# Kernel optimization log

Hardware: AMD Instinct MI355X
Metric: run time of the kernel (lower is better)

The kernel has to match this reference:

```python
import jax, jax.numpy as jnp
import numpy as np

ANCHORS = np.array([[10,13],[16,30],[33,23],[30,61],[62,45],[59,119],[116,90],[156,198],[373,326]], np.float32)
ANCHOR_MASK = [[6, 7, 8], [3, 4, 5], [0, 1, 2]]
INPUT_SHAPE = np.array([416, 416], np.float32)  # (h, w)
NUM_CLASSES = 80
EPS = 1e-7


def _bce(pred, target):
    # clip_by_tensor + binary cross entropy, as in the torch module
    p = jnp.clip(pred, EPS, 1.0 - EPS)
    return -target * jnp.log(p) - (1.0 - target) * jnp.log(1.0 - p)


def _box_iou(b1, b2):
    # b1: (..., 1, 4), b2: (..., n, 4), center-format xywh (normalized)
    b1_xy, b1_wh = b1[..., :2], b1[..., 2:4]
    b2_xy, b2_wh = b2[..., :2], b2[..., 2:4]
    b1_min, b1_max = b1_xy - b1_wh / 2.0, b1_xy + b1_wh / 2.0
    b2_min, b2_max = b2_xy - b2_wh / 2.0, b2_xy + b2_wh / 2.0
    inter_wh = jnp.maximum(jnp.minimum(b1_max, b2_max) - jnp.maximum(b1_min, b2_min), 0.0)
    inter = inter_wh[..., 0] * inter_wh[..., 1]
    a1 = b1_wh[..., 0] * b1_wh[..., 1]
    a2 = b2_wh[..., 0] * b2_wh[..., 1]
    return inter / (a1 + a2 - inter)


def _decode(y_pred, anchors):
    # y_pred: (b, 3*(5+C), h, w) -> raw: (b, 3, h, w, 5+C)
    b, _, h, w = y_pred.shape
    raw = y_pred.reshape(b, 3, 5 + NUM_CLASSES, h, w).transpose(0, 1, 3, 4, 2)
    gy, gx = jnp.meshgrid(jnp.arange(h, dtype=y_pred.dtype), jnp.arange(w, dtype=y_pred.dtype), indexing='ij')
    grid_xy = jnp.stack([gx, gy], axis=-1)  # (h, w, 2)
    pred_xy = jax.nn.sigmoid(raw[..., 0:2])
    pred_wh = raw[..., 2:4]                 # raw tw, th (MSE'd against log target)
    pred_conf = jax.nn.sigmoid(raw[..., 4:5])
    pred_class = jax.nn.sigmoid(raw[..., 5:])
    # decoded, normalized boxes for IoU-based negative mining
    box_xy = (pred_xy + grid_xy) / jnp.array([w, h], y_pred.dtype)
    box_wh = jnp.exp(pred_wh) * anchors.reshape(3, 1, 1, 2) / jnp.asarray(INPUT_SHAPE[::-1].copy())
    pred_box = jnp.concatenate([box_xy, box_wh], axis=-1)  # (b,3,h,w,4)
    return grid_xy, pred_box, pred_xy, pred_wh, pred_conf, pred_class


def _layer_loss(y_pred, y_true, target, anchors):
    b, _, h, w = y_pred.shape
    grid_xy, pred_box, pred_xy, pred_wh, pred_conf, pred_class = _decode(y_pred, anchors)
    object_mask = y_true[..., 4:5]
    true_xy = y_true[..., 0:2] * jnp.array([h, w], y_pred.dtype) - grid_xy
    true_wh = jnp.log(y_true[..., 2:4] * jnp.asarray(INPUT_SHAPE[::-1].copy()) / anchors.reshape(3, 1, 1, 2))
    true_wh = jnp.where(object_mask > 0, true_wh, jnp.zeros_like(true_wh))
    loss_scale = 2.0 - y_true[..., 2:3] * y_true[..., 3:4]
    # negative mask: every grid/anchor prediction vs all true boxes of its image (vectorized over batch)
    iou = _box_iou(pred_box[:, :, :, :, None, :], target[:, None, None, None, :, :4])  # (b,3,h,w,n)
    best_iou = jnp.max(iou, axis=-1)
    neg = (best_iou < 0.5).astype(y_pred.dtype)[..., None]
    neg_mask = (1.0 - object_mask) * neg
    loss_xy = jnp.sum(object_mask * loss_scale * _bce(pred_xy, true_xy))
    loss_wh = jnp.sum(object_mask * loss_scale * 0.5 * (pred_wh - true_wh) ** 2)
    conf_bce = _bce(pred_conf, object_mask)
    loss_conf = jnp.sum(object_mask * conf_bce) + jnp.sum(neg_mask * conf_bce)
    loss_cls = jnp.sum(object_mask * _bce(pred_class, y_true[..., 5:]))
    return loss_xy + loss_wh + loss_conf + loss_cls


def setup_inputs() -> dict:
    key = jax.random.key(0)
    ks = jax.random.split(key, 7)
    grids = [13, 26, 52]
    b, n = 32, 20
    inp = {}
    for i, g in enumerate(grids):
        inp[f'y_pred{i}'] = jax.random.normal(ks[i], (b, 3 * (5 + NUM_CLASSES), g, g), jnp.float32)
        # y_true values in (0.05, 0.95): keeps log(true_wh) and 1/y_true grads bounded
        inp[f'y_true{i}'] = 0.05 + 0.9 * jax.random.uniform(ks[3 + i], (b, 3, g, g, 5 + NUM_CLASSES), jnp.float32)
    inp['target'] = 0.05 + 0.9 * jax.random.uniform(ks[6], (b, n, 5), jnp.float32)
    return inp


def reference(y_pred0, y_pred1, y_pred2, y_true0, y_true1, y_true2, target):
    total = jnp.zeros((), jnp.float32)
    for yp, yt, mask in ((y_pred0, y_true0, ANCHOR_MASK[0]),
                         (y_pred1, y_true1, ANCHOR_MASK[1]),
                         (y_pred2, y_true2, ANCHOR_MASK[2])):
        total = total + _layer_loss(yp, yt, target, jnp.asarray(ANCHORS[mask]))
    return total
```

## Files before the change

kernel.cpp:

```cpp
#include <hip/hip_runtime.h>
#include <math.h>

#define BLOCK 256
#define NB0 64
#define NB1 254
#define NB2 1014
#define NBLOCKS (NB0 + NB1 + NB2)

__constant__ float c_anch[9][2] = {
    {116.f, 90.f}, {156.f, 198.f}, {373.f, 326.f},
    { 30.f, 61.f}, { 62.f,  45.f}, { 59.f, 119.f},
    { 10.f, 13.f}, { 16.f,  30.f}, { 33.f,  23.f}
};

__device__ __forceinline__ float softplusf(float x) {
    float ax = fabsf(x);
    return fmaxf(x, 0.f) + __logf(1.f + __expf(-ax));
}

__device__ __forceinline__ float sigmoidf(float x) {
    return __fdividef(1.f, 1.f + __expf(-x));
}

__global__ __launch_bounds__(BLOCK) void yolo_loss_main(
    const float* __restrict__ p0, const float* __restrict__ p1, const float* __restrict__ p2,
    const float* __restrict__ t0, const float* __restrict__ t1, const float* __restrict__ t2,
    const float* __restrict__ tgt, float* __restrict__ out)
{
    int blk = blockIdx.x;
    const float* pred;
    const float* tru;
    int layer, g, cells, bbase;
    if (blk < NB0)            { layer = 0; pred = p0; tru = t0; g = 13; cells = 16224;  bbase = 0; }
    else if (blk < NB0 + NB1) { layer = 1; pred = p1; tru = t1; g = 26; cells = 64896;  bbase = NB0; }
    else                      { layer = 2; pred = p2; tru = t2; g = 52; cells = 259584; bbase = NB0 + NB1; }

    const int tid  = threadIdx.x;
    const int w    = tid >> 6;
    const int lane = tid & 63;
    const int cellbase = (blk - bbase) * BLOCK;
    const int wbase = cellbase + w * 64;
    const int idx   = wbase + lane;
    const bool valid = idx < cells;

    __shared__ float lds[4][16][68];

    const int hw = g * g;
    const float* pb = pred;
    float aw = 1.f, ah = 1.f, gx = 0.f, gy = 0.f;
    int b = 0;
    if (valid) {
        int ij = idx % hw;
        int a  = (idx / hw) % 3;
        b      = idx / (3 * hw);
        int i  = ij / g;
        int j  = ij - i * g;
        pb = pred + (size_t)((b * 3 + a) * 85) * hw + ij;
        aw = c_anch[layer * 3 + a][0];
        ah = c_anch[layer * 3 + a][1];
        gx = (float)j; gy = (float)i;
    }
    const float gf = (float)g;

    const float* src = tru + (size_t)wbase * 85;

    float acc = 0.f;
    float cls = 0.f;
    float mask = 0.f;

#pragma unroll
    for (int k = 0; k < 16; k++) {
        int e  = k * 64 + lane;
        int cl = e >> 4, c = e & 15;
        if (wbase + cl < cells)
            lds[w][c][cl] = src[(size_t)cl * 85 + c];
    }

    if (valid) {
        float y0 = lds[w][0][lane], y1 = lds[w][1][lane];
        float y2 = lds[w][2][lane], y3 = lds[w][3][lane];
        mask = lds[w][4][lane];

        float r0 = pb[0];
        float r1 = pb[hw];
        float r2 = pb[2 * hw];
        float r3 = pb[3 * hw];
        float r4 = pb[4 * hw];

        float true_x = y0 * gf - gx;
        float true_y = y1 * gf - gy;
        float ls = 2.f - y2 * y3;
        float lxy = (softplusf(r0) - true_x * r0) + (softplusf(r1) - true_y * r1);
        acc += mask * ls * lxy;

        float tw = __logf(y2 * (416.f / aw));
        float th = __logf(y3 * (416.f / ah));
        float dw = r2 - tw, dh = r3 - th;
        acc += mask * ls * 0.5f * (dw * dw + dh * dh);

        float cbce = softplusf(r4) - mask * r4;
        float sx = sigmoidf(r0);
        float sy = sigmoidf(r1);
        float bx = __fdividef(sx + gx, gf);
        float by = __fdividef(sy + gy, gf);
        float bw = __expf(r2) * aw * (1.f / 416.f);
        float bh = __expf(r3) * ah * (1.f / 416.f);
        float a1 = bw * bh;
        float b1minx = bx - 0.5f * bw, b1maxx = bx + 0.5f * bw;
        float b1miny = by - 0.5f * bh, b1maxy = by + 0.5f * bh;

        const float* tg = tgt + b * 20 * 5;
        float best = 0.f;
#pragma unroll 4
        for (int k = 0; k < 20; k++) {
            float tx  = tg[k * 5 + 0];
            float ty  = tg[k * 5 + 1];
            float tww = tg[k * 5 + 2];
            float thh = tg[k * 5 + 3];
            float iw = fminf(b1maxx, tx + 0.5f * tww) - fmaxf(b1minx, tx - 0.5f * tww);
            float ih = fminf(b1maxy, ty + 0.5f * thh) - fmaxf(b1miny, ty - 0.5f * thh);
            iw = fmaxf(iw, 0.f);
            ih = fmaxf(ih, 0.f);
            float inter = iw * ih;
            float iou = __fdividef(inter, a1 + tww * thh - inter);
            best = fmaxf(best, iou);
        }
        float neg = (best < 0.5f) ? 1.f : 0.f;
        acc += mask * cbce + (1.f - mask) * neg * cbce;

#pragma unroll
        for (int c = 5; c < 16; c++) {
            float x = pb[c * hw];
            float t = lds[w][c][lane];
            cls += softplusf(x) - t * x;
        }
    }

#pragma unroll
    for (int c0 = 16; c0 < 80; c0 += 16) {
#pragma unroll
        for (int k = 0; k < 16; k++) {
            int e  = k * 64 + lane;
            int cl = e >> 4, c = e & 15;
            if (wbase + cl < cells)
                lds[w][c][cl] = src[(size_t)cl * 85 + c0 + c];
        }
        if (valid) {
#pragma unroll
            for (int c = 0; c < 16; c++) {
                float x = pb[(c0 + c) * hw];
                float t = lds[w][c][lane];
                cls += softplusf(x) - t * x;
            }
        }
    }

#pragma unroll
    for (int k = 0; k < 5; k++) {
        int e  = k * 64 + lane;
        int cl = e / 5, c = e - cl * 5;
        if (wbase + cl < cells)
            lds[w][c][cl] = src[(size_t)cl * 85 + 80 + c];
    }
    if (valid) {
#pragma unroll
        for (int c = 0; c < 5; c++) {
            float x = pb[(80 + c) * hw];
            float t = lds[w][c][lane];
            cls += softplusf(x) - t * x;
        }
        acc += mask * cls;
    }

    for (int off = 32; off > 0; off >>= 1)
        acc += __shfl_down(acc, off, 64);
    __shared__ float sh[BLOCK / 64];
    if (lane == 0)
        sh[w] = acc;
    __syncthreads();
    if (tid == 0) {
        float s = 0.f;
        for (int wv = 0; wv < BLOCK / 64; wv++) s += sh[wv];
        atomicAdd(out, s);
    }
}

extern "C" void kernel_launch(void* const* d_in, const int* in_sizes, int n_in,
                              void* d_out, int out_size, void* d_ws, size_t ws_size,
                              hipStream_t stream) {
    const float* p0  = (const float*)d_in[0];
    const float* t0  = (const float*)d_in[1];
    const float* p1  = (const float*)d_in[2];
    const float* t1  = (const float*)d_in[3];
    const float* p2  = (const float*)d_in[4];
    const float* t2  = (const float*)d_in[5];
    const float* tgt = (const float*)d_in[6];

    hipMemsetAsync(d_out, 0, sizeof(float), stream);
    yolo_loss_main<<<NBLOCKS, BLOCK, 0, stream>>>(p0, p1, p2, t0, t1, t2, tgt, (float*)d_out);
}
```

Baseline: 301.7 us.

## Process four cells per lane with vectorized loads in single-wave blocks

Changes blocks to a single 64-lane wavefront in which each lane handles four consecutive cells of layers 1 and 2. Prediction planes are read with float4 loads, and y_true rows are staged through a transposing LDS tile using float4 reads. Layer 0 (13x13, where a 4-cell group can straddle plane boundaries) moves to a scalar per-thread path that reads y_true directly. The block-level LDS reduction and barrier are replaced by one atomic per wave, which raises the atomic count on the single output. The aim is wider memory transactions and amortized IoU target loads, at the cost of more registers per lane and more atomics.

```diff
diff --git a/kernel.cpp b/kernel.cpp
--- a/kernel.cpp
+++ b/kernel.cpp
@@ -1,11 +1,12 @@
 #include <hip/hip_runtime.h>
 #include <math.h>
 
-#define BLOCK 256
-#define NB0 64
-#define NB1 254
-#define NB2 1014
-#define NBLOCKS (NB0 + NB1 + NB2)
+typedef float f4 __attribute__((ext_vector_type(4)));
+
+#define NL2 1014
+#define NL1 254
+#define NL0 254
+#define NBLOCKS (NL2 + NL1 + NL0)
 
 __constant__ float c_anch[9][2] = {
     {116.f, 90.f}, {156.f, 198.f}, {373.f, 326.f},
@@ -17,172 +18,245 @@
     float ax = fabsf(x);
     return fmaxf(x, 0.f) + __logf(1.f + __expf(-ax));
 }
-
 __device__ __forceinline__ float sigmoidf(float x) {
     return __fdividef(1.f, 1.f + __expf(-x));
 }
 
-__global__ __launch_bounds__(BLOCK) void yolo_loss_main(
+__global__ __launch_bounds__(64) void yolo_loss_main(
     const float* __restrict__ p0, const float* __restrict__ p1, const float* __restrict__ p2,
     const float* __restrict__ t0, const float* __restrict__ t1, const float* __restrict__ t2,
     const float* __restrict__ tgt, float* __restrict__ out)
 {
-    int blk = blockIdx.x;
-    const float* pred;
-    const float* tru;
-    int layer, g, cells, bbase;
-    if (blk < NB0)            { layer = 0; pred = p0; tru = t0; g = 13; cells = 16224;  bbase = 0; }
-    else if (blk < NB0 + NB1) { layer = 1; pred = p1; tru = t1; g = 26; cells = 64896;  bbase = NB0; }
-    else                      { layer = 2; pred = p2; tru = t2; g = 52; cells = 259584; bbase = NB0 + NB1; }
-
-    const int tid  = threadIdx.x;
-    const int w    = tid >> 6;
-    const int lane = tid & 63;
-    const int cellbase = (blk - bbase) * BLOCK;
-    const int wbase = cellbase + w * 64;
-    const int idx   = wbase + lane;
-    const bool valid = idx < cells;
-
-    __shared__ float lds[4][16][68];
-
-    const int hw = g * g;
-    const float* pb = pred;
-    float aw = 1.f, ah = 1.f, gx = 0.f, gy = 0.f;
-    int b = 0;
-    if (valid) {
-        int ij = idx % hw;
-        int a  = (idx / hw) % 3;
-        b      = idx / (3 * hw);
-        int i  = ij / g;
-        int j  = ij - i * g;
-        pb = pred + (size_t)((b * 3 + a) * 85) * hw + ij;
-        aw = c_anch[layer * 3 + a][0];
-        ah = c_anch[layer * 3 + a][1];
-        gx = (float)j; gy = (float)i;
+    __shared__ float lds[16][260];
+
+    const int blk  = blockIdx.x;
+    const int lane = threadIdx.x;
+    float acc = 0.f;
+
+    if (blk < NL2 + NL1) {
+        const float* pred; const float* tru;
+        int hw, cells, base, arow;
+        int plane, ij0, cell0;
+        float gf;
+        float gxv[4], gyv[4];
+        if (blk < NL2) {
+            pred = p2; tru = t2; hw = 2704; cells = 259584; arow = 6; gf = 52.f;
+            base  = blk * 256;
+            cell0 = base + 4 * lane;
+            plane = cell0 / 2704; ij0 = cell0 - plane * 2704;
+#pragma unroll
+            for (int s = 0; s < 4; s++) { int ij = ij0 + s; int i = ij / 52; gyv[s] = (float)i; gxv[s] = (float)(ij - i * 52); }
+        } else {
+            pred = p1; tru = t1; hw = 676; cells = 64896; arow = 3; gf = 26.f;
+            base  = (blk - NL2) * 256;
+            cell0 = base + 4 * lane;
+            plane = cell0 / 676; ij0 = cell0 - plane * 676;
+#pragma unroll
+            for (int s = 0; s < 4; s++) { int ij = ij0 + s; int i = ij / 26; gyv[s] = (float)i; gxv[s] = (float)(ij - i * 26); }
+        }
+        const bool valid = cell0 < cells;
+        const int aIdx = plane % 3;
+        const int bIdx = plane / 3;
+        const float* pb = pred + (size_t)plane * 85 * hw + ij0;
+        const float aw = c_anch[arow + aIdx][0];
+        const float ah = c_anch[arow + aIdx][1];
+        const char* tbase = (const char*)tru + (size_t)base * 340;
+
+        f4 clsv = {0.f, 0.f, 0.f, 0.f};
+        float m4[4] = {0.f, 0.f, 0.f, 0.f};
+
+#pragma unroll
+        for (int k = 0; k < 16; k++) {
+            int u = k * 64 + lane;
+            int cell = u >> 2, q = u & 3;
+            if (base + cell < cells) {
+                f4 v = *(const f4*)(tbase + (size_t)cell * 340 + q * 16);
+                lds[4*q+0][cell] = v.x;
+                lds[4*q+1][cell] = v.y;
+                lds[4*q+2][cell] = v.z;
+                lds[4*q+3][cell] = v.w;
+            }
+        }
+        if (valid) {
+            f4 y0 = *(const f4*)&lds[0][4*lane];
+            f4 y1 = *(const f4*)&lds[1][4*lane];
+            f4 y2 = *(const f4*)&lds[2][4*lane];
+            f4 y3 = *(const f4*)&lds[3][4*lane];
+            f4 ym = *(const f4*)&lds[4][4*lane];
+            f4 r0 = *(const f4*)(pb);
+            f4 r1 = *(const f4*)(pb + (size_t)hw);
+            f4 r2 = *(const f4*)(pb + 2*(size_t)hw);
+            f4 r3 = *(const f4*)(pb + 3*(size_t)hw);
+            f4 r4 = *(const f4*)(pb + 4*(size_t)hw);
+
+            float cb[4], bminx[4], bmaxx[4], bminy[4], bmaxy[4], area[4], best[4];
+#pragma unroll
+            for (int s = 0; s < 4; s++) {
+                float R0 = r0[s], R1 = r1[s], R2 = r2[s], R3 = r3[s], R4 = r4[s];
+                float Y0 = y0[s], Y1 = y1[s], Y2 = y2[s], Y3 = y3[s], M = ym[s];
+                m4[s] = M;
+                float gx = gxv[s], gy = gyv[s];
+                float tx = Y0 * gf - gx, ty = Y1 * gf - gy;
+                float ls = 2.f - Y2 * Y3;
+                acc += M * ls * ((softplusf(R0) - tx * R0) + (softplusf(R1) - ty * R1));
+                float tw = __logf(Y2 * (416.f / aw));
+                float th = __logf(Y3 * (416.f / ah));
+                float dw = R2 - tw, dh = R3 - th;
+                acc += M * ls * 0.5f * (dw * dw + dh * dh);
+                cb[s] = softplusf(R4) - M * R4;
+                float sx = sigmoidf(R0), sy = sigmoidf(R1);
+                float bx = __fdividef(sx + gx, gf), by = __fdividef(sy + gy, gf);
+                float bw = __expf(R2) * aw * (1.f / 416.f);
+                float bh = __expf(R3) * ah * (1.f / 416.f);
+                area[s]  = bw * bh;
+                bminx[s] = bx - 0.5f * bw; bmaxx[s] = bx + 0.5f * bw;
+                bminy[s] = by - 0.5f * bh; bmaxy[s] = by + 0.5f * bh;
+                best[s]  = 0.f;
+            }
+            const float* tg = tgt + bIdx * 100;
+#pragma unroll 4
+            for (int k = 0; k < 20; k++) {
+                float tx = tg[5*k], ty = tg[5*k+1], tw = tg[5*k+2], th = tg[5*k+3];
+                float tminx = tx - 0.5f * tw, tmaxx = tx + 0.5f * tw;
+                float tminy = ty - 0.5f * th, tmaxy = ty + 0.5f * th;
+                float a2 = tw * th;
+#pragma unroll
+                for (int s = 0; s < 4; s++) {
+                    float iw = fmaxf(fminf(bmaxx[s], tmaxx) - fmaxf(bminx[s], tminx), 0.f);
+                    float ih = fmaxf(fminf(bmaxy[s], tmaxy) - fmaxf(bminy[s], tminy), 0.f);
+                    float inter = iw * ih;
+                    best[s] = fmaxf(best[s], __fdividef(inter, area[s] + a2 - inter));
+                }
+            }
+#pragma unroll
+            for (int s = 0; s < 4; s++) {
+                float neg = (best[s] < 0.5f) ? 1.f : 0.f;
+                acc += m4[s] * cb[s] + (1.f - m4[s]) * neg * cb[s];
+            }
+#pragma unroll
+            for (int c = 5; c < 16; c++) {
+                f4 tv = *(const f4*)&lds[c][4*lane];
+                f4 xv = *(const f4*)(pb + (size_t)c * hw);
+                f4 sp;
+                sp.x = softplusf(xv.x); sp.y = softplusf(xv.y);
+                sp.z = softplusf(xv.z); sp.w = softplusf(xv.w);
+                clsv += sp - tv * xv;
+            }
+        }
+
+        for (int cc = 16; cc < 80; cc += 16) {
+            const char* tc = tbase + cc * 4;
+#pragma unroll
+            for (int k = 0; k < 16; k++) {
+                int u = k * 64 + lane;
+                int cell = u >> 2, q = u & 3;
+                if (base + cell < cells) {
+                    f4 v = *(const f4*)(tc + (size_t)cell * 340 + q * 16);
+                    lds[4*q+0][cell] = v.x;
+                    lds[4*q+1][cell] = v.y;
+                    lds[4*q+2][cell] = v.z;
+                    lds[4*q+3][cell] = v.w;
+                }
+            }
+            if (valid) {
+#pragma unroll
+                for (int c = 0; c < 16; c++) {
+                    f4 tv = *(const f4*)&lds[c][4*lane];
+                    f4 xv = *(const f4*)(pb + (size_t)(cc + c) * hw);
+                    f4 sp;
+                    sp.x = softplusf(xv.x); sp.y = softplusf(xv.y);
+                    sp.z = softplusf(xv.z); sp.w = softplusf(xv.w);
+                    clsv += sp - tv * xv;
+                }
+            }
+        }
+
+        {
+            const char* tc = tbase + 320;
+#pragma unroll
+            for (int k = 0; k < 20; k++) {
+                int u = k * 64 + lane;
+                int cell = u / 5, c = u - cell * 5;
+                if (base + cell < cells)
+                    lds[c][cell] = *(const float*)(tc + (size_t)cell * 340 + c * 4);
+            }
+            if (valid) {
+#pragma unroll
+                for (int c = 0; c < 5; c++) {
+                    f4 tv = *(const f4*)&lds[c][4*lane];
+                    f4 xv = *(const f4*)(pb + (size_t)(80 + c) * hw);
+                    f4 sp;
+                    sp.x = softplusf(xv.x); sp.y = softplusf(xv.y);
+                    sp.z = softplusf(xv.z); sp.w = softplusf(xv.w);
+                    clsv += sp - tv * xv;
+                }
+            }
+        }
+
+        if (valid)
+            acc += m4[0]*clsv.x + m4[1]*clsv.y + m4[2]*clsv.z + m4[3]*clsv.w;
+
+    } else {
+        int t = (blk - NL2 - NL1) * 64 + lane;
+        if (t < 16224) {
+            int ij = t % 169;
+            int a  = (t / 169) % 3;
+            int b  = t / 507;
+            int i  = ij / 13;
+            int j  = ij - i * 13;
+            const float* pb = p0 + (size_t)((b * 3 + a) * 85) * 169 + ij;
+            const float* tb = t0 + (size_t)((b * 3 + a) * 169 + ij) * 85;
+
+            float r0 = pb[0], r1 = pb[169], r2 = pb[338], r3 = pb[507], r4 = pb[676];
+            float y0 = tb[0], y1 = tb[1], y2 = tb[2], y3 = tb[3], mask = tb[4];
+            float aw = c_anch[a][0], ah = c_anch[a][1];
+            float gx = (float)j, gy = (float)i;
+
+            float tx = y0 * 13.f - gx, ty = y1 * 13.f - gy;
+            float ls = 2.f - y2 * y3;
+            acc += mask * ls * ((softplusf(r0) - tx * r0) + (softplusf(r1) - ty * r1));
+            float tw = __logf(y2 * (416.f / aw));
+            float th = __logf(y3 * (416.f / ah));
+            float dw = r2 - tw, dh = r3 - th;
+            acc += mask * ls * 0.5f * (dw * dw + dh * dh);
+            float cbce = softplusf(r4) - mask * r4;
+
+            float sx = sigmoidf(r0), sy = sigmoidf(r1);
+            float bx = __fdividef(sx + gx, 13.f), by = __fdividef(sy + gy, 13.f);
+            float bw = __expf(r2) * aw * (1.f / 416.f);
+            float bh = __expf(r3) * ah * (1.f / 416.f);
+            float a1 = bw * bh;
+            float b1minx = bx - 0.5f * bw, b1maxx = bx + 0.5f * bw;
+            float b1miny = by - 0.5f * bh, b1maxy = by + 0.5f * bh;
+            const float* tg = tgt + b * 100;
+            float bestv = 0.f;
+#pragma unroll 4
+            for (int k = 0; k < 20; k++) {
+                float px = tg[5*k], py = tg[5*k+1], pw = tg[5*k+2], ph = tg[5*k+3];
+                float iw = fmaxf(fminf(b1maxx, px + 0.5f*pw) - fmaxf(b1minx, px - 0.5f*pw), 0.f);
+                float ih = fmaxf(fminf(b1maxy, py + 0.5f*ph) - fmaxf(b1miny, py - 0.5f*ph), 0.f);
+                float inter = iw * ih;
+                bestv = fmaxf(bestv, __fdividef(inter, a1 + pw * ph - inter));
+            }
+            float neg = (bestv < 0.5f) ? 1.f : 0.f;
+            acc += mask * cbce + (1.f - mask) * neg * cbce;
+
+            float cls = 0.f;
+#pragma unroll 8
+            for (int c = 0; c < 80; c++) {
+                float x = pb[(5 + c) * 169];
+                float tt = tb[5 + c];
+                cls += softplusf(x) - tt * x;
+            }
+            acc += mask * cls;
+        }
     }
-    const float gf = (float)g;
-
-    const float* src = tru + (size_t)wbase * 85;
-
-    float acc = 0.f;
-    float cls = 0.f;
-    float mask = 0.f;
-
-#pragma unroll
-    for (int k = 0; k < 16; k++) {
-        int e  = k * 64 + lane;
-        int cl = e >> 4, c = e & 15;
-        if (wbase + cl < cells)
-            lds[w][c][cl] = src[(size_t)cl * 85 + c];
-    }
-
-    if (valid) {
-        float y0 = lds[w][0][lane], y1 = lds[w][1][lane];
-        float y2 = lds[w][2][lane], y3 = lds[w][3][lane];
-        mask = lds[w][4][lane];
-
-        float r0 = pb[0];
-        float r1 = pb[hw];
-        float r2 = pb[2 * hw];
-        float r3 = pb[3 * hw];
-        float r4 = pb[4 * hw];
-
-        float true_x = y0 * gf - gx;
-        float true_y = y1 * gf - gy;
-        float ls = 2.f - y2 * y3;
-        float lxy = (softplusf(r0) - true_x * r0) + (softplusf(r1) - true_y * r1);
-        acc += mask * ls * lxy;
-
-        float tw = __logf(y2 * (416.f / aw));
-        float th = __logf(y3 * (416.f / ah));
-        float dw = r2 - tw, dh = r3 - th;
-        acc += mask * ls * 0.5f * (dw * dw + dh * dh);
-
-        float cbce = softplusf(r4) - mask * r4;
-        float sx = sigmoidf(r0);
-        float sy = sigmoidf(r1);
-        float bx = __fdividef(sx + gx, gf);
-        float by = __fdividef(sy + gy, gf);
-        float bw = __expf(r2) * aw * (1.f / 416.f);
-        float bh = __expf(r3) * ah * (1.f / 416.f);
-        float a1 = bw * bh;
-        float b1minx = bx - 0.5f * bw, b1maxx = bx + 0.5f * bw;
-        float b1miny = by - 0.5f * bh, b1maxy = by + 0.5f * bh;
-
-        const float* tg = tgt + b * 20 * 5;
-        float best = 0.f;
-#pragma unroll 4
-        for (int k = 0; k < 20; k++) {
-            float tx  = tg[k * 5 + 0];
-            float ty  = tg[k * 5 + 1];
-            float tww = tg[k * 5 + 2];
-            float thh = tg[k * 5 + 3];
-            float iw = fminf(b1maxx, tx + 0.5f * tww) - fmaxf(b1minx, tx - 0.5f * tww);
-            float ih = fminf(b1maxy, ty + 0.5f * thh) - fmaxf(b1miny, ty - 0.5f * thh);
-            iw = fmaxf(iw, 0.f);
-            ih = fmaxf(ih, 0.f);
-            float inter = iw * ih;
-            float iou = __fdividef(inter, a1 + tww * thh - inter);
-            best = fmaxf(best, iou);
-        }
-        float neg = (best < 0.5f) ? 1.f : 0.f;
-        acc += mask * cbce + (1.f - mask) * neg * cbce;
-
-#pragma unroll
-        for (int c = 5; c < 16; c++) {
-            float x = pb[c * hw];
-            float t = lds[w][c][lane];
-            cls += softplusf(x) - t * x;
-        }
-    }
-
-#pragma unroll
-    for (int c0 = 16; c0 < 80; c0 += 16) {
-#pragma unroll
-        for (int k = 0; k < 16; k++) {
-            int e  = k * 64 + lane;
-            int cl = e >> 4, c = e & 15;
-            if (wbase + cl < cells)
-                lds[w][c][cl] = src[(size_t)cl * 85 + c0 + c];
-        }
-        if (valid) {
-#pragma unroll
-            for (int c = 0; c < 16; c++) {
-                float x = pb[(c0 + c) * hw];
-                float t = lds[w][c][lane];
-                cls += softplusf(x) - t * x;
-            }
-        }
-    }
-
-#pragma unroll
-    for (int k = 0; k < 5; k++) {
-        int e  = k * 64 + lane;
-        int cl = e / 5, c = e - cl * 5;
-        if (wbase + cl < cells)
-            lds[w][c][cl] = src[(size_t)cl * 85 + 80 + c];
-    }
-    if (valid) {
-#pragma unroll
-        for (int c = 0; c < 5; c++) {
-            float x = pb[(80 + c) * hw];
-            float t = lds[w][c][lane];
-            cls += softplusf(x) - t * x;
-        }
-        acc += mask * cls;
-    }
-
+
+#pragma unroll
     for (int off = 32; off > 0; off >>= 1)
         acc += __shfl_down(acc, off, 64);
-    __shared__ float sh[BLOCK / 64];
     if (lane == 0)
-        sh[w] = acc;
-    __syncthreads();
-    if (tid == 0) {
-        float s = 0.f;
-        for (int wv = 0; wv < BLOCK / 64; wv++) s += sh[wv];
-        atomicAdd(out, s);
-    }
+        atomicAdd(out, acc);
 }
 
 extern "C" void kernel_launch(void* const* d_in, const int* in_sizes, int n_in,
@@ -197,5 +271,5 @@
     const float* tgt = (const float*)d_in[6];
 
     hipMemsetAsync(d_out, 0, sizeof(float), stream);
-    yolo_loss_main<<<NBLOCKS, BLOCK, 0, stream>>>(p0, p1, p2, t0, t1, t2, tgt, (float*)d_out);
-}
+    yolo_loss_main<<<NBLOCKS, 64, 0, stream>>>(p0, p1, p2, t0, t1, t2, tgt, (float*)d_out);
+}
```

Measured after the change: 292.8 us. 3.0% less time.
